# Performance work log

Measured on AMD Instinct MI355X. Metric: run time of the kernel, lower is better.

## Reference

```python
import jax, jax.numpy as jnp
import numpy as np

D_MODEL, N_STATE, L_MAX, BATCH = 256, 64, 2048, 16

def _to_c(x):
    return jax.lax.complex(x[..., 0], x[..., 1])

def setup_inputs() -> dict:
    key = jax.random.key(0)
    k_u, k_ct_r, k_ct_i, k_step = jax.random.split(key, 4)
    n, d = N_STATE, D_MODEL
    # --- HiPPO DPLR init (numpy, matches torch hippo_dplr) ---
    P = np.sqrt(1.0 + 2.0 * np.arange(1, n + 1, dtype=np.float64))
    A = np.tril(np.outer(P, P)) - np.diag(np.arange(1, n + 1, dtype=np.float64))
    A = -A
    p = 0.5 * np.sqrt(2.0 * np.arange(1, n + 1, dtype=np.float64) + 1.0)
    Ap = (A + np.outer(p, p)).astype(np.complex64)
    lam, V = np.linalg.eig(Ap)
    p_rot = V.conj().T @ p.astype(np.complex64)
    p_ri = np.stack([p_rot.real, p_rot.imag], -1).astype(np.float32)          # (n,2)
    lambda_ri = np.stack([lam.real, lam.imag], -1).astype(np.float32)         # (n,2)
    # --- B init: sqrt(2k+1), repeated over channels, zero imag ---
    B_r = np.sqrt(2.0 * np.arange(1, n + 1) + 1.0).astype(np.float32)
    B_ri = np.stack([np.tile(B_r, (d, 1)), np.zeros((d, n), np.float32)], -1) # (d,n,2)
    # --- Ct: xavier-normal complex ---
    std = float(np.sqrt(2.0 / (d + n)))
    Ct_r = jax.random.normal(k_ct_r, (d, n), jnp.float32) * (std / np.sqrt(2.0))
    Ct_i = jax.random.normal(k_ct_i, (d, n), jnp.float32) * (std / np.sqrt(2.0))
    Ct_ri = jnp.stack([Ct_r, Ct_i], -1)                                        # (d,n,2)
    Dp = jnp.ones((1, 1, d), jnp.float32)
    log_step = jax.random.uniform(k_step, (d,), jnp.float32) * (
        np.log(0.1) - np.log(0.001)) + np.log(0.001)
    u = jax.random.normal(k_u, (BATCH, L_MAX, d), jnp.float32)
    return {"u": u, "p_ri": jnp.asarray(p_ri), "lambda_ri": jnp.asarray(lambda_ri),
            "B_ri": jnp.asarray(B_ri), "Ct_ri": Ct_ri, "Dp": Dp, "log_step": log_step}

def reference(u, p_ri, lambda_ri, B_ri, Ct_ri, Dp, log_step):
    p = _to_c(p_ri)          # (n,)
    lam = _to_c(lambda_ri)   # (n,)
    B = _to_c(B_ri)          # (d,n)
    Ct = _to_c(Ct_ri)        # (d,n)
    L = u.shape[1]
    omega = jnp.exp(2j * jnp.pi * jnp.arange(L) / L).astype(jnp.complex64)  # (L,)
    step = jnp.exp(log_step)                                               # (d,)
    g = (2.0 / step)[:, None] * ((1.0 - omega) / (1.0 + omega))[None, :]   # (d,L)
    c = 2.0 / (1.0 + omega)                                                # (L,)
    inv = 1.0 / (g[:, :, None] - lam[None, None, :])                       # (d,L,n)
    k00 = jnp.einsum('dn,dln->dl', Ct.conj() * B, inv)
    k01 = jnp.einsum('dn,dln->dl', Ct.conj() * p[None, :], inv)
    k10 = jnp.einsum('dn,dln->dl', p.conj()[None, :] * B, inv)
    k11 = jnp.einsum('n,dln->dl', p.conj() * p, inv)
    at_roots = c[None, :] * (k00 - k01 * k10 / (1.0 + k11))                # (d,L)
    out = jnp.fft.ifft(at_roots, n=L, axis=-1)
    order = jnp.concatenate([jnp.zeros((1,), jnp.int32), jnp.arange(L - 1, 0, -1)])
    K = out[:, order].real[None]                                           # (1,d,L)
    # causal FFT convolution
    ud = jnp.fft.rfft(jnp.pad(u, ((0, 0), (0, L), (0, 0))), axis=1)        # (B,L+1,d)
    Kd = jnp.fft.rfft(jnp.pad(K, ((0, 0), (0, 0), (0, L))), axis=-1)       # (1,d,L+1)
    y = jnp.fft.irfft(jnp.transpose(ud, (0, 2, 1)) * Kd, axis=-1)[..., :L]
    y = jnp.transpose(y, (0, 2, 1)).astype(u.dtype)                        # (B,L,d)
    return y + Dp * u
```

## Files before the change

### kernel.cpp

```cpp
#include <hip/hip_runtime.h>
#include <math.h>

#define LLEN   2048
#define NFFT   4096
#define DMODEL 256
#define NSTATE 64
#define NBATCH 16
#define PI_F   3.14159265358979323846f

#define PADIDX(a) ((a) + ((a) >> 4))
#define LDSN2 (LLEN + (LLEN >> 4))
#define KSTRIDE 2056

#define SWZIDX(a) ((a) ^ (((a) >> 4) & 15))

__device__ inline float frcp(float x) { return __builtin_amdgcn_rcpf(x); }

#define RADIX4(ar0,ai0,ar1,ai1,ar2,ai2,ar3,ai3,S) do {                      \
    float s0r=(ar0)+(ar2), s0i=(ai0)+(ai2);                                 \
    float s1r=(ar0)-(ar2), s1i=(ai0)-(ai2);                                 \
    float s2r=(ar1)+(ar3), s2i=(ai1)+(ai3);                                 \
    float s3r=(ar1)-(ar3), s3i=(ai1)-(ai3);                                 \
    (ar0)=s0r+s2r; (ai0)=s0i+s2i;                                           \
    (ar2)=s0r-s2r; (ai2)=s0i-s2i;                                           \
    (ar1)=s1r-(S)*s3i; (ai1)=s1i+(S)*s3r;                                   \
    (ar3)=s1r+(S)*s3i; (ai3)=s1i-(S)*s3r;                                   \
} while (0)

template<int SIGN>
__device__ inline void dft16(float xr[16], float xi[16]) {
    const float S = (float)SIGN;
    const float C1 = 0.9238795325112867f, S1 = 0.3826834323650898f;
    const float C2 = 0.7071067811865476f;
    RADIX4(xr[0],xi[0], xr[4],xi[4], xr[8],xi[8],  xr[12],xi[12], S);
    RADIX4(xr[1],xi[1], xr[5],xi[5], xr[9],xi[9],  xr[13],xi[13], S);
    RADIX4(xr[2],xi[2], xr[6],xi[6], xr[10],xi[10],xr[14],xi[14], S);
    RADIX4(xr[3],xi[3], xr[7],xi[7], xr[11],xi[11],xr[15],xi[15], S);
#define TW(idx, wr_, wi_) { float tr = xr[idx]*(wr_) - xi[idx]*(wi_);       \
    xi[idx] = xr[idx]*(wi_) + xi[idx]*(wr_); xr[idx] = tr; }
    TW(5,  C1,  S*S1);
    TW(6,  C2,  S*C2);
    TW(7,  S1,  S*C1);
    TW(9,  C2,  S*C2);
    TW(10, 0.f, S);
    TW(11, -C2, S*C2);
    TW(13, S1,  S*C1);
    TW(14, -C2, S*C2);
    TW(15, -C1, -S*S1);
#undef TW
    RADIX4(xr[0],xi[0],  xr[1],xi[1],  xr[2],xi[2],  xr[3],xi[3],  S);
    RADIX4(xr[4],xi[4],  xr[5],xi[5],  xr[6],xi[6],  xr[7],xi[7],  S);
    RADIX4(xr[8],xi[8],  xr[9],xi[9],  xr[10],xi[10],xr[11],xi[11],S);
    RADIX4(xr[12],xi[12],xr[13],xi[13],xr[14],xi[14],xr[15],xi[15],S);
}

template<int SIGN>
__device__ inline void dft8(float xr[8], float xi[8]) {
    const float S = (float)SIGN;
    const float C2 = 0.7071067811865476f;
    RADIX4(xr[0],xi[0], xr[2],xi[2], xr[4],xi[4], xr[6],xi[6], S);
    RADIX4(xr[1],xi[1], xr[3],xi[3], xr[5],xi[5], xr[7],xi[7], S);
    { float tr = xr[3]*C2 - xi[3]*(S*C2); xi[3] = xr[3]*(S*C2) + xi[3]*C2; xr[3] = tr; }
    { float tr = -S*xi[5]; xi[5] = S*xr[5]; xr[5] = tr; }
    { float tr = xr[7]*(-C2) - xi[7]*(S*C2); xi[7] = xr[7]*(S*C2) + xi[7]*(-C2); xr[7] = tr; }
    float br[8], bi[8];
#pragma unroll
    for (int k = 0; k < 4; ++k) {
        br[k]   = xr[2*k] + xr[2*k+1]; bi[k]   = xi[2*k] + xi[2*k+1];
        br[k+4] = xr[2*k] - xr[2*k+1]; bi[k+4] = xi[2*k] - xi[2*k+1];
    }
#pragma unroll
    for (int k = 0; k < 8; ++k) { xr[k] = br[k]; xi[k] = bi[k]; }
}

template<int SIGN>
__device__ inline void tw_apply16(float xr[16], float xi[16], float ang) {
    float wr[16], wi[16];
    __sincosf(ang, &wi[1], &wr[1]);
#pragma unroll
    for (int k = 1; k < 8; ++k) {
        wr[2*k]   = wr[k]*wr[k] - wi[k]*wi[k];
        wi[2*k]   = 2.f * wr[k] * wi[k];
        wr[2*k+1] = wr[k]*wr[k+1] - wi[k]*wi[k+1];
        wi[2*k+1] = wr[k]*wi[k+1] + wi[k]*wr[k+1];
    }
#pragma unroll
    for (int t = 1; t < 16; ++t) {
        float tr = xr[t]*wr[t] - xi[t]*wi[t];
        xi[t] = xr[t]*wi[t] + xi[t]*wr[t];
        xr[t] = tr;
    }
}

template<int SIGN, int M, int L, bool PRUNE>
__device__ inline void stage16(float2* X, int j, bool active) {
    float xr[16], xi[16];
    const int p = j & (L - 1);
    if (active) {
#pragma unroll
        for (int t = 0; t < 16; ++t) {
            float2 v = X[PADIDX(j + t * M)];
            xr[t] = v.x; xi[t] = v.y;
        }
        tw_apply16<SIGN>(xr, xi, ((float)SIGN * 2.f * PI_F / (float)(16 * L)) * (float)p);
        dft16<SIGN>(xr, xi);
    }
    __syncthreads();
    if (active) {
        const int base = 16 * j - 15 * p;
#pragma unroll
        for (int k0 = 0; k0 < 4; ++k0)
#pragma unroll
            for (int k2 = 0; k2 < 4; ++k2) {
                const int u = k0 + 4 * k2;
                if (!PRUNE || u < 8) {
                    const int a = base + u * L;
                    X[PADIDX(a)] = make_float2(xr[4*k0+k2], xi[4*k0+k2]);
                }
            }
    }
    __syncthreads();
}

template<int SIGN>
__device__ inline void fft2048_f2(float2* X, int tid) {
    float xr[8], xi[8];
#pragma unroll
    for (int t = 0; t < 8; ++t) {
        float2 v = X[PADIDX(tid + t * 256)];
        xr[t] = v.x; xi[t] = v.y;
    }
    dft8<SIGN>(xr, xi);
    __syncthreads();
#pragma unroll
    for (int u = 0; u < 8; ++u)
        X[PADIDX(8 * tid + u)] = make_float2(xr[u], xi[u]);
    __syncthreads();
    stage16<SIGN, 128, 8,   false>(X, tid, tid < 128);
    stage16<SIGN, 128, 128, false>(X, tid, tid < 128);
}

template<int SIGN, int M, int L, bool PRUNE>
__device__ inline void stage16s(float2* X, int j) {
    float xr[16], xi[16];
    const int p = j & (L - 1);
#pragma unroll
    for (int t = 0; t < 16; ++t) {
        float2 v = X[SWZIDX(j + t * M)];
        xr[t] = v.x; xi[t] = v.y;
    }
    tw_apply16<SIGN>(xr, xi, ((float)SIGN * 2.f * PI_F / (float)(16 * L)) * (float)p);
    dft16<SIGN>(xr, xi);
    __syncthreads();
    const int base = 16 * j - 15 * p;
#pragma unroll
    for (int k0 = 0; k0 < 4; ++k0)
#pragma unroll
        for (int k2 = 0; k2 < 4; ++k2) {
            const int u = k0 + 4 * k2;
            if (!PRUNE || u < 8) {
                const int a = base + u * L;
                X[SWZIDX(a)] = make_float2(xr[4*k0+k2], xi[4*k0+k2]);
            }
        }
    __syncthreads();
}

template<int SIGN, bool PRUNE>
__device__ inline void fft4096_swz_from_regs(float2* X, int tid,
                                             float xr[16], float xi[16]) {
    dft16<SIGN>(xr, xi);
#pragma unroll
    for (int k0 = 0; k0 < 4; ++k0)
#pragma unroll
        for (int k2 = 0; k2 < 4; ++k2)
            X[SWZIDX(16 * tid + k0 + 4 * k2)] = make_float2(xr[4*k0+k2], xi[4*k0+k2]);
    __syncthreads();
    stage16s<SIGN, 256, 16,  false>(X, tid);
    stage16s<SIGN, 256, 256, PRUNE>(X, tid);
}

template<int SIGN, bool PRUNE>
__device__ inline void fft4096_swz(float2* X, int tid) {
    float xr[16], xi[16];
#pragma unroll
    for (int t = 0; t < 16; ++t) {
        float2 v = X[SWZIDX(tid + t * 256)];
        xr[t] = v.x; xi[t] = v.y;
    }
    dft16<SIGN>(xr, xi);
    __syncthreads();
#pragma unroll
    for (int k0 = 0; k0 < 4; ++k0)
#pragma unroll
        for (int k2 = 0; k2 < 4; ++k2)
            X[SWZIDX(16 * tid + k0 + 4 * k2)] = make_float2(xr[4*k0+k2], xi[4*k0+k2]);
    __syncthreads();
    stage16s<SIGN, 256, 16,  false>(X, tid);
    stage16s<SIGN, 256, 256, PRUNE>(X, tid);
}

__global__ __launch_bounds__(256) void k_ar(const float* __restrict__ p_ri,
                                            const float* __restrict__ lambda_ri,
                                            const float* __restrict__ B_ri,
                                            const float* __restrict__ Ct_ri,
                                            const float* __restrict__ log_step,
                                            float2* __restrict__ ar_out) {
    __shared__ float4 c0[NSTATE], c1[NSTATE];
    __shared__ float2 lam[NSTATE];
    const int d = blockIdx.x >> 1;
    const int lbase = (blockIdx.x & 1) << 10;
    const int tid = threadIdx.x;
    if (tid < NSTATE) {
        const int n = tid;
        const float px = p_ri[2*n], py = p_ri[2*n+1];
        lam[n] = make_float2(lambda_ri[2*n], lambda_ri[2*n+1]);
        const float Bx = B_ri[(d*NSTATE+n)*2], By = B_ri[(d*NSTATE+n)*2+1];
        const float Cx = Ct_ri[(d*NSTATE+n)*2], Cy = Ct_ri[(d*NSTATE+n)*2+1];
        c0[n] = make_float4(Cx*Bx + Cy*By, Cx*By - Cy*Bx,
                            Cx*px + Cy*py, Cx*py - Cy*px);
        c1[n] = make_float4(px*Bx + py*By, px*By - py*Bx, px*px + py*py, 0.f);
    }
    __syncthreads();

    const float tos = 2.f * __expf(-log_step[d]);
    float gx[4], gy[4], ccx[4], ccy[4];
    float k00x[4], k00y[4], k01x[4], k01y[4];
    float k10x[4], k10y[4], k11x[4], k11y[4];
#pragma unroll
    for (int j = 0; j < 4; ++j) {
        const int l = lbase + tid + (j << 8);
        float sn, cs;
        sincosf(2.f * PI_F * (float)l / (float)LLEN, &sn, &cs);
        const float opx = 1.f + cs, opy = sn;
        const float omx = 1.f - cs, omy = -sn;
        const float inv_op = frcp(opx*opx + opy*opy);
        gx[j] = tos * (omx*opx + omy*opy) * inv_op;
        gy[j] = tos * (omy*opx - omx*opy) * inv_op;
        ccx[j] = 2.f * opx * inv_op; ccy[j] = -2.f * opy * inv_op;
        k00x[j]=0.f; k00y[j]=0.f; k01x[j]=0.f; k01y[j]=0.f;
        k10x[j]=0.f; k10y[j]=0.f; k11x[j]=0.f; k11y[j]=0.f;
    }
    for (int n = 0; n < NSTATE; ++n) {
        const float2 lm = lam[n];
        const float4 a = c0[n];
        const float4 b = c1[n];
#pragma unroll
        for (int j = 0; j < 4; ++j) {
            const float dx = gx[j] - lm.x, dy = gy[j] - lm.y;
            const float idn = frcp(dx*dx + dy*dy);
            const float ix = dx * idn, iy = -dy * idn;
            k00x[j] += a.x*ix - a.y*iy;  k00y[j] += a.x*iy + a.y*ix;
            k01x[j] += a.z*ix - a.w*iy;  k01y[j] += a.z*iy + a.w*ix;
            k10x[j] += b.x*ix - b.y*iy;  k10y[j] += b.x*iy + b.y*ix;
            k11x[j] += b.z*ix;           k11y[j] += b.z*iy;
        }
    }
#pragma unroll
    for (int j = 0; j < 4; ++j) {
        const float nx = k01x[j]*k10x[j] - k01y[j]*k10y[j];
        const float ny = k01x[j]*k10y[j] + k01y[j]*k10x[j];
        const float dpx = 1.f + k11x[j], dpy = k11y[j];
        const float idq = frcp(dpx*dpx + dpy*dpy);
        const float qx = (nx*dpx + ny*dpy) * idq;
        const float qy = (ny*dpx - nx*dpy) * idq;
        const float rx = k00x[j] - qx, ry = k00y[j] - qy;
        ar_out[(size_t)d * LLEN + lbase + tid + (j << 8)] =
            make_float2(ccx[j]*rx - ccy[j]*ry, ccx[j]*ry + ccy[j]*rx);
    }
}

__global__ __launch_bounds__(256, 4) void k_mix(const float2* __restrict__ a_in,
                                                float2* __restrict__ Hc) {
    __shared__ float2 X[LDSN2];
    const int tid = threadIdx.x;
    const int d = blockIdx.x;
    const float isc = 1.f / (float)NFFT;
    const float4* a4 = (const float4*)(a_in + (size_t)d * LLEN);
#pragma unroll
    for (int k = 0; k < 4; ++k) {
        const int v = tid + k * 256;
        const float4 w = a4[v];
        X[PADIDX(2 * v)]     = make_float2(w.x, w.y);
        X[PADIDX(2 * v + 1)] = make_float2(w.z, w.w);
    }
    __syncthreads();

    float2* H = Hc + (size_t)d * KSTRIDE;
    for (int m = tid; m <= 1024; m += 256) {
        const float2 am = X[PADIDX(m)];
        const float2 an = X[PADIDX((LLEN - m) & (LLEN - 1))];
        H[2 * m] = make_float2((an.x + am.x) * 0.5f * isc,
                               (an.y - am.y) * 0.5f * isc);
    }
    fft2048_f2<-1>(X, tid);

#pragma unroll
    for (int k = 0; k < 8; ++k) {
        const int j = tid + k * 256;
        const int q = PADIDX(j);
        const float Kj = X[q].x * (1.f / (float)LLEN);
        float snj, csj;
        __sincosf(-PI_F * (float)j * (1.f / 2048.f), &snj, &csj);
        X[q] = make_float2(Kj * csj, Kj * snj);
    }
    __syncthreads();
    fft2048_f2<-1>(X, tid);

    for (int m = tid; m < 1024; m += 256) {
        const float2 w = X[PADIDX(m)];
        H[2 * m + 1] = make_float2(w.x * isc, w.y * isc);
    }
}

__device__ inline void pointwise2s(float2* __restrict__ X,
                                   const float2* __restrict__ Ha,
                                   const float2* __restrict__ Hb, int tid) {
    for (int f = tid; f <= NFFT / 2; f += 256) {
        const int fb = (NFFT - f) & (NFFT - 1);
        const float2 Za = X[SWZIDX(f)], Zb = X[SWZIDX(fb)];
        const float xax = 0.5f * (Za.x + Zb.x), xay = 0.5f * (Za.y - Zb.y);
        const float xbx = 0.5f * (Za.y + Zb.y), xby = -0.5f * (Za.x - Zb.x);
        const float2 A = Ha[f], B = Hb[f];
        const float yax = xax*A.x - xay*A.y, yay = xax*A.y + xay*A.x;
        const float ybx = xbx*B.x - xby*B.y, yby = xbx*B.y + xby*B.x;
        X[SWZIDX(f)] = make_float2(yax - yby, yay + ybx);
        if (fb != f)
            X[SWZIDX(fb)] = make_float2(yax + yby, ybx - yay);
    }
    __syncthreads();
}

__global__ __launch_bounds__(256, 8) void k_fused(const float* __restrict__ u,
                                                  const float2* __restrict__ Hc,
                                                  const float* __restrict__ Dp,
                                                  float* __restrict__ out) {
    __shared__ float2 X[NFFT];
    const int i = blockIdx.x;
    const int x = i & 7;
    const int s = i >> 3;
    const int b  = s >> 4;
    const int cp = (x << 4) | (s & 15);
    const int ch = cp * 2;
    const int tid = threadIdx.x;

    const float* ub = u + (size_t)b * (LLEN * DMODEL) + ch;

    float xr[16], xi[16];
#pragma unroll
    for (int k = 0; k < 8; ++k) {
        const float2 v = *(const float2*)(ub + (size_t)(tid + k * 256) * DMODEL);
        xr[k] = v.x; xi[k] = v.y;
    }
#pragma unroll
    for (int k = 8; k < 16; ++k) { xr[k] = 0.f; xi[k] = 0.f; }

    fft4096_swz_from_regs<-1, false>(X, tid, xr, xi);
    pointwise2s(X, Hc + (size_t)ch * KSTRIDE, Hc + (size_t)(ch + 1) * KSTRIDE, tid);
    fft4096_swz<+1, true>(X, tid);

    const float2 dp = *(const float2*)(Dp + ch);
    float* ob = out + (size_t)b * (LLEN * DMODEL) + ch;
#pragma unroll
    for (int k = 0; k < 8; ++k) {
        const int t = tid + k * 256;
        const float2 v  = X[SWZIDX(t)];
        const float2 uu = *(const float2*)(ub + (size_t)t * DMODEL);
        *(float2*)(ob + (size_t)t * DMODEL) =
            make_float2(v.x + dp.x * uu.x, v.y + dp.y * uu.y);
    }
}

extern "C" void kernel_launch(void* const* d_in, const int* in_sizes, int n_in,
                              void* d_out, int out_size, void* d_ws, size_t ws_size,
                              hipStream_t stream) {
    const float* u         = (const float*)d_in[0];
    const float* p_ri      = (const float*)d_in[1];
    const float* lambda_ri = (const float*)d_in[2];
    const float* B_ri      = (const float*)d_in[3];
    const float* Ct_ri     = (const float*)d_in[4];
    const float* Dp        = (const float*)d_in[5];
    const float* log_step  = (const float*)d_in[6];
    float* out = (float*)d_out;

    float2* Hc = (float2*)d_ws;
    float2* a  = (float2*)((char*)d_ws + (size_t)DMODEL * KSTRIDE * sizeof(float2));

    k_ar   <<<DMODEL * 2, 256, 0, stream>>>(p_ri, lambda_ri, B_ri, Ct_ri, log_step, a);
    k_mix  <<<DMODEL, 256, 0, stream>>>(a, Hc);
    k_fused<<<NBATCH * (DMODEL / 2), 256, 0, stream>>>(u, Hc, Dp, out);
}
```

Baseline: 185.1 us.

## Stage 8-channel u tile in LDS for wide coalesced loads and stores

Measured after the change: 198.4 us. 7.2% more time.

```diff
diff --git a/kernel.cpp b/kernel.cpp
--- a/kernel.cpp
+++ b/kernel.cpp
@@ -200,6 +200,24 @@
     stage16s<SIGN, 256, 256, PRUNE>(X, tid);
 }
 
+__device__ inline void pointwise2s(float2* __restrict__ X,
+                                   const float2* __restrict__ Ha,
+                                   const float2* __restrict__ Hb, int tid) {
+    for (int f = tid; f <= NFFT / 2; f += 256) {
+        const int fb = (NFFT - f) & (NFFT - 1);
+        const float2 Za = X[SWZIDX(f)], Zb = X[SWZIDX(fb)];
+        const float xax = 0.5f * (Za.x + Zb.x), xay = 0.5f * (Za.y - Zb.y);
+        const float xbx = 0.5f * (Za.y + Zb.y), xby = -0.5f * (Za.x - Zb.x);
+        const float2 A = Ha[f], B = Hb[f];
+        const float yax = xax*A.x - xay*A.y, yay = xax*A.y + xay*A.x;
+        const float ybx = xbx*B.x - xby*B.y, yby = xbx*B.y + xby*B.x;
+        X[SWZIDX(f)] = make_float2(yax - yby, yay + ybx);
+        if (fb != f)
+            X[SWZIDX(fb)] = make_float2(yax + yby, ybx - yay);
+    }
+    __syncthreads();
+}
+
 __global__ __launch_bounds__(256) void k_ar(const float* __restrict__ p_ri,
                                             const float* __restrict__ lambda_ri,
                                             const float* __restrict__ B_ri,
@@ -313,61 +331,87 @@
     }
 }
 
-__device__ inline void pointwise2s(float2* __restrict__ X,
-                                   const float2* __restrict__ Ha,
-                                   const float2* __restrict__ Hb, int tid) {
-    for (int f = tid; f <= NFFT / 2; f += 256) {
-        const int fb = (NFFT - f) & (NFFT - 1);
-        const float2 Za = X[SWZIDX(f)], Zb = X[SWZIDX(fb)];
-        const float xax = 0.5f * (Za.x + Zb.x), xay = 0.5f * (Za.y - Zb.y);
-        const float xbx = 0.5f * (Za.y + Zb.y), xby = -0.5f * (Za.x - Zb.x);
-        const float2 A = Ha[f], B = Hb[f];
-        const float yax = xax*A.x - xay*A.y, yay = xax*A.y + xay*A.x;
-        const float ybx = xbx*B.x - xby*B.y, yby = xbx*B.y + xby*B.x;
-        X[SWZIDX(f)] = make_float2(yax - yby, yay + ybx);
-        if (fb != f)
-            X[SWZIDX(fb)] = make_float2(yax + yby, ybx - yay);
-    }
-    __syncthreads();
-}
-
-__global__ __launch_bounds__(256, 8) void k_fused(const float* __restrict__ u,
-                                                  const float2* __restrict__ Hc,
-                                                  const float* __restrict__ Dp,
-                                                  float* __restrict__ out) {
-    __shared__ float2 X[NFFT];
+__global__ __launch_bounds__(512, 2) void k_fused8(const float* __restrict__ u,
+                                                   const float2* __restrict__ Hc,
+                                                   const float* __restrict__ Dp,
+                                                   float* __restrict__ out) {
+    __shared__ float tile[8 * LLEN];
+    __shared__ float2 Xbuf[2][NFFT];
     const int i = blockIdx.x;
     const int x = i & 7;
-    const int s = i >> 3;
-    const int b  = s >> 4;
-    const int cp = (x << 4) | (s & 15);
-    const int ch = cp * 2;
-    const int tid = threadIdx.x;
-
-    const float* ub = u + (size_t)b * (LLEN * DMODEL) + ch;
-
-    float xr[16], xi[16];
-#pragma unroll
-    for (int k = 0; k < 8; ++k) {
-        const float2 v = *(const float2*)(ub + (size_t)(tid + k * 256) * DMODEL);
-        xr[k] = v.x; xi[k] = v.y;
-    }
-#pragma unroll
-    for (int k = 8; k < 16; ++k) { xr[k] = 0.f; xi[k] = 0.f; }
-
-    fft4096_swz_from_regs<-1, false>(X, tid, xr, xi);
-    pointwise2s(X, Hc + (size_t)ch * KSTRIDE, Hc + (size_t)(ch + 1) * KSTRIDE, tid);
-    fft4096_swz<+1, true>(X, tid);
-
-    const float2 dp = *(const float2*)(Dp + ch);
-    float* ob = out + (size_t)b * (LLEN * DMODEL) + ch;
-#pragma unroll
-    for (int k = 0; k < 8; ++k) {
-        const int t = tid + k * 256;
-        const float2 v  = X[SWZIDX(t)];
-        const float2 uu = *(const float2*)(ub + (size_t)t * DMODEL);
-        *(float2*)(ob + (size_t)t * DMODEL) =
-            make_float2(v.x + dp.x * uu.x, v.y + dp.y * uu.y);
+    const int s_ = i >> 3;
+    const int cg = (x << 2) | (s_ & 3);
+    const int b  = s_ >> 2;
+    const int tid  = threadIdx.x;
+    const int sq   = tid >> 8;
+    const int tq   = tid & 255;
+    float2* X = Xbuf[sq];
+
+    const float* ub = u + (size_t)b * (LLEN * DMODEL) + cg * 8;
+    {
+        const int row0 = tid >> 1;
+        const int c4   = (tid & 1) * 4;
+#pragma unroll
+        for (int k = 0; k < 8; ++k) {
+            const int t = row0 + k * 256;
+            const float4 v = *(const float4*)(ub + (size_t)t * DMODEL + c4);
+            tile[(c4 + 0) * LLEN + t] = v.x;
+            tile[(c4 + 1) * LLEN + t] = v.y;
+            tile[(c4 + 2) * LLEN + t] = v.z;
+            tile[(c4 + 3) * LLEN + t] = v.w;
+        }
+    }
+    __syncthreads();
+
+#pragma unroll
+    for (int r = 0; r < 2; ++r) {
+        const int p   = 2 * r + sq;
+        const int chA = cg * 8 + 2 * p;
+        const float* tA = tile + (2 * p) * LLEN;
+        const float* tB = tile + (2 * p + 1) * LLEN;
+
+        float xr[16], xi[16];
+#pragma unroll
+        for (int k = 0; k < 8; ++k) {
+            const int t = tq + k * 256;
+            xr[k] = tA[t];
+            xi[k] = tB[t];
+        }
+#pragma unroll
+        for (int k = 8; k < 16; ++k) { xr[k] = 0.f; xi[k] = 0.f; }
+
+        fft4096_swz_from_regs<-1, false>(X, tq, xr, xi);
+        pointwise2s(X, Hc + (size_t)chA * KSTRIDE,
+                       Hc + (size_t)(chA + 1) * KSTRIDE, tq);
+        fft4096_swz<+1, true>(X, tq);
+
+        const float dpA = Dp[chA], dpB = Dp[chA + 1];
+        float* wA = tile + (2 * p) * LLEN;
+        float* wB = tile + (2 * p + 1) * LLEN;
+#pragma unroll
+        for (int k = 0; k < 8; ++k) {
+            const int t = tq + k * 256;
+            const float2 v = X[SWZIDX(t)];
+            wA[t] = v.x + dpA * wA[t];
+            wB[t] = v.y + dpB * wB[t];
+        }
+        __syncthreads();
+    }
+
+    float* ob = out + (size_t)b * (LLEN * DMODEL) + cg * 8;
+    {
+        const int row0 = tid >> 1;
+        const int c4   = (tid & 1) * 4;
+#pragma unroll
+        for (int k = 0; k < 8; ++k) {
+            const int t = row0 + k * 256;
+            float4 o;
+            o.x = tile[(c4 + 0) * LLEN + t];
+            o.y = tile[(c4 + 1) * LLEN + t];
+            o.z = tile[(c4 + 2) * LLEN + t];
+            o.w = tile[(c4 + 3) * LLEN + t];
+            *(float4*)(ob + (size_t)t * DMODEL + c4) = o;
+        }
     }
 }
 
@@ -386,7 +430,7 @@
     float2* Hc = (float2*)d_ws;
     float2* a  = (float2*)((char*)d_ws + (size_t)DMODEL * KSTRIDE * sizeof(float2));
 
-    k_ar   <<<DMODEL * 2, 256, 0, stream>>>(p_ri, lambda_ri, B_ri, Ct_ri, log_step, a);
-    k_mix  <<<DMODEL, 256, 0, stream>>>(a, Hc);
-    k_fused<<<NBATCH * (DMODEL / 2), 256, 0, stream>>>(u, Hc, Dp, out);
-}
+    k_ar    <<<DMODEL * 2, 256, 0, stream>>>(p_ri, lambda_ri, B_ri, Ct_ri, log_step, a);
+    k_mix   <<<DMODEL, 256, 0, stream>>>(a, Hc);
+    k_fused8<<<NBATCH * (DMODEL / 8), 512, 0, stream>>>(u, Hc, Dp, out);
+}
```

## Transpose input to channel-major and pair batches per channel in convolution

Applied to the files above, without the earlier changes.

Measured after the change: 175.6 us. -5.1%, faster.

```diff
diff --git a/kernel.cpp b/kernel.cpp
--- a/kernel.cpp
+++ b/kernel.cpp
@@ -270,10 +270,33 @@
     }
 }
 
-__global__ __launch_bounds__(256, 4) void k_mix(const float2* __restrict__ a_in,
+__global__ __launch_bounds__(256, 4) void k_mix(const float* __restrict__ u,
+                                                const float2* __restrict__ a_in,
+                                                float* __restrict__ ut,
                                                 float2* __restrict__ Hc) {
     __shared__ float2 X[LDSN2];
     const int tid = threadIdx.x;
+
+    if (blockIdx.x >= DMODEL) {
+        const int blk = blockIdx.x - DMODEL;
+        const int bt0 = (blk & 1023) * 32;
+        const int ch0 = (blk >> 10) * 32;
+        float* tile = (float*)X;
+        const int tx = tid & 31, ty = tid >> 5;
+#pragma unroll
+        for (int k = 0; k < 4; ++k) {
+            const int r = ty + 8 * k;
+            tile[r * 33 + tx] = u[(size_t)(bt0 + r) * DMODEL + ch0 + tx];
+        }
+        __syncthreads();
+#pragma unroll
+        for (int k = 0; k < 4; ++k) {
+            const int r = ty + 8 * k;
+            ut[(size_t)(ch0 + r) * (NBATCH * LLEN) + bt0 + tx] = tile[tx * 33 + r];
+        }
+        return;
+    }
+
     const int d = blockIdx.x;
     const float isc = 1.f / (float)NFFT;
     const float4* a4 = (const float4*)(a_in + (size_t)d * LLEN);
@@ -313,61 +336,82 @@
     }
 }
 
-__device__ inline void pointwise2s(float2* __restrict__ X,
-                                   const float2* __restrict__ Ha,
-                                   const float2* __restrict__ Hb, int tid) {
+__global__ __launch_bounds__(256, 8) void k_conv(const float* __restrict__ ut,
+                                                 const float2* __restrict__ Hc,
+                                                 const float* __restrict__ Dp,
+                                                 float* __restrict__ yt) {
+    __shared__ float2 X[NFFT];
+    const int bid = blockIdx.x;
+    const int x = bid & 7;
+    const int s = bid >> 3;
+    const int ch = (x << 5) | (s & 31);
+    const int pair = s >> 5;
+    const int tid = threadIdx.x;
+
+    const float* u0 = ut + (size_t)ch * (NBATCH * LLEN) + (size_t)(2 * pair) * LLEN;
+    const float* u1 = u0 + LLEN;
+
+    float xr[16], xi[16];
+#pragma unroll
+    for (int k = 0; k < 8; ++k) {
+        xr[k] = u0[tid + k * 256];
+        xi[k] = u1[tid + k * 256];
+    }
+#pragma unroll
+    for (int k = 8; k < 16; ++k) { xr[k] = 0.f; xi[k] = 0.f; }
+
+    fft4096_swz_from_regs<-1, false>(X, tid, xr, xi);
+
+    const float2* H = Hc + (size_t)ch * KSTRIDE;
     for (int f = tid; f <= NFFT / 2; f += 256) {
         const int fb = (NFFT - f) & (NFFT - 1);
         const float2 Za = X[SWZIDX(f)], Zb = X[SWZIDX(fb)];
-        const float xax = 0.5f * (Za.x + Zb.x), xay = 0.5f * (Za.y - Zb.y);
-        const float xbx = 0.5f * (Za.y + Zb.y), xby = -0.5f * (Za.x - Zb.x);
-        const float2 A = Ha[f], B = Hb[f];
-        const float yax = xax*A.x - xay*A.y, yay = xax*A.y + xay*A.x;
-        const float ybx = xbx*B.x - xby*B.y, yby = xbx*B.y + xby*B.x;
-        X[SWZIDX(f)] = make_float2(yax - yby, yay + ybx);
-        if (fb != f)
-            X[SWZIDX(fb)] = make_float2(yax + yby, ybx - yay);
-    }
-    __syncthreads();
-}
-
-__global__ __launch_bounds__(256, 8) void k_fused(const float* __restrict__ u,
-                                                  const float2* __restrict__ Hc,
-                                                  const float* __restrict__ Dp,
-                                                  float* __restrict__ out) {
-    __shared__ float2 X[NFFT];
-    const int i = blockIdx.x;
-    const int x = i & 7;
-    const int s = i >> 3;
-    const int b  = s >> 4;
-    const int cp = (x << 4) | (s & 15);
-    const int ch = cp * 2;
+        const float u0x = 0.5f * (Za.x + Zb.x), u0y = 0.5f * (Za.y - Zb.y);
+        const float u1x = 0.5f * (Za.y + Zb.y), u1y = -0.5f * (Za.x - Zb.x);
+        const float2 Ha = H[f];
+        const float y0x = u0x*Ha.x - u0y*Ha.y, y0y = u0x*Ha.y + u0y*Ha.x;
+        const float y1x = u1x*Ha.x - u1y*Ha.y, y1y = u1x*Ha.y + u1y*Ha.x;
+        X[SWZIDX(f)] = make_float2(y0x - y1y, y0y + y1x);
+        if (fb != f) {
+            const float Hbx = Ha.x, Hby = -Ha.y;
+            const float z0x = u0x*Hbx + u0y*Hby, z0y = u0x*Hby - u0y*Hbx;
+            const float z1x = u1x*Hbx + u1y*Hby, z1y = u1x*Hby - u1y*Hbx;
+            X[SWZIDX(fb)] = make_float2(z0x - z1y, z0y + z1x);
+        }
+    }
+    __syncthreads();
+    fft4096_swz<+1, true>(X, tid);
+
+    const float dp = Dp[ch];
+    float* y0o = yt + (size_t)ch * (NBATCH * LLEN) + (size_t)(2 * pair) * LLEN;
+    float* y1o = y0o + LLEN;
+    for (int i = tid; i < LLEN; i += 256) {
+        const float2 v = X[SWZIDX(i)];
+        y0o[i] = v.x + dp * u0[i];
+        y1o[i] = v.y + dp * u1[i];
+    }
+}
+
+__global__ __launch_bounds__(256) void k_post(const float* __restrict__ yt,
+                                              float* __restrict__ out) {
+    __shared__ float tile[32][33];
+    const int bt0 = blockIdx.x * 32, ch0 = blockIdx.y * 32;
     const int tid = threadIdx.x;
-
-    const float* ub = u + (size_t)b * (LLEN * DMODEL) + ch;
-
-    float xr[16], xi[16];
-#pragma unroll
-    for (int k = 0; k < 8; ++k) {
-        const float2 v = *(const float2*)(ub + (size_t)(tid + k * 256) * DMODEL);
-        xr[k] = v.x; xi[k] = v.y;
-    }
-#pragma unroll
-    for (int k = 8; k < 16; ++k) { xr[k] = 0.f; xi[k] = 0.f; }
-
-    fft4096_swz_from_regs<-1, false>(X, tid, xr, xi);
-    pointwise2s(X, Hc + (size_t)ch * KSTRIDE, Hc + (size_t)(ch + 1) * KSTRIDE, tid);
-    fft4096_swz<+1, true>(X, tid);
-
-    const float2 dp = *(const float2*)(Dp + ch);
-    float* ob = out + (size_t)b * (LLEN * DMODEL) + ch;
-#pragma unroll
-    for (int k = 0; k < 8; ++k) {
-        const int t = tid + k * 256;
-        const float2 v  = X[SWZIDX(t)];
-        const float2 uu = *(const float2*)(ub + (size_t)t * DMODEL);
-        *(float2*)(ob + (size_t)t * DMODEL) =
-            make_float2(v.x + dp.x * uu.x, v.y + dp.y * uu.y);
+    {
+        const int r = tid >> 3, c = (tid & 7) * 4;
+        const float4 v = *(const float4*)&yt[(size_t)(ch0 + r) * (NBATCH * LLEN) + bt0 + c];
+        tile[r][c] = v.x; tile[r][c+1] = v.y; tile[r][c+2] = v.z; tile[r][c+3] = v.w;
+    }
+    __syncthreads();
+    {
+        const int r = tid >> 3, c4 = (tid & 7) * 4;
+        const size_t idx = (size_t)(bt0 + r) * DMODEL + ch0 + c4;
+        float4 o;
+        o.x = tile[c4 + 0][r];
+        o.y = tile[c4 + 1][r];
+        o.z = tile[c4 + 2][r];
+        o.w = tile[c4 + 3][r];
+        *(float4*)&out[idx] = o;
     }
 }
 
@@ -384,9 +428,13 @@
     float* out = (float*)d_out;
 
     float2* Hc = (float2*)d_ws;
-    float2* a  = (float2*)((char*)d_ws + (size_t)DMODEL * KSTRIDE * sizeof(float2));
-
-    k_ar   <<<DMODEL * 2, 256, 0, stream>>>(p_ri, lambda_ri, B_ri, Ct_ri, log_step, a);
-    k_mix  <<<DMODEL, 256, 0, stream>>>(a, Hc);
-    k_fused<<<NBATCH * (DMODEL / 2), 256, 0, stream>>>(u, Hc, Dp, out);
-}
+    char*   wb = (char*)d_ws + (size_t)DMODEL * KSTRIDE * sizeof(float2);
+    float2* a  = (float2*)wb;
+    float*  yt = (float*)wb;
+    float*  ut = out;
+
+    k_ar  <<<DMODEL * 2, 256, 0, stream>>>(p_ri, lambda_ri, B_ri, Ct_ri, log_step, a);
+    k_mix <<<DMODEL + 8192, 256, 0, stream>>>(u, a, ut, Hc);
+    k_conv<<<DMODEL * (NBATCH / 2), 256, 0, stream>>>(ut, Hc, Dp, yt);
+    k_post<<<dim3(NBATCH * LLEN / 32, DMODEL / 32), 256, 0, stream>>>(yt, out);
+}
```
